# Performance work log

Hardware: AMD Instinct MI355X
Metric: run time of the kernel (lower is better)

Reference implementation:

```python
import jax, jax.numpy as jnp
import numpy as np

NUM_FIELDS = 26

def setup_inputs() -> dict:
    key = jax.random.key(0)
    ks = jax.random.split(key, 8)
    B, F, D, V, d, af = 4096, NUM_FIELDS, 13, 100000, 64, 64
    return {
        "sparse_feat": jax.random.randint(ks[0], (B, F), 0, V, dtype=jnp.int32),
        "dense_feat": jax.random.uniform(ks[1], (B, D), dtype=jnp.float32),
        "embed_table": jax.random.normal(ks[2], (V, d), dtype=jnp.float32) * 0.05,
        "lin_table": jax.random.normal(ks[3], (V,), dtype=jnp.float32) * 0.05,
        "w_dense": jax.random.normal(ks[4], (D,), dtype=jnp.float32) * 0.1,
        "bias": jnp.zeros((1,), dtype=jnp.float32),
        "W1": jax.random.normal(ks[5], (d, af), dtype=jnp.float32) * (1.0 / np.sqrt(d)),
        "b1": jnp.zeros((af,), dtype=jnp.float32),
        "w2": jax.random.normal(ks[6], (af,), dtype=jnp.float32) * (1.0 / np.sqrt(af)),
        "p": jax.random.normal(ks[7], (d,), dtype=jnp.float32) * (1.0 / np.sqrt(d)),
    }

def reference(sparse_feat, dense_feat, embed_table, lin_table, w_dense, bias, W1, b1, w2, p):
    # Embedding lookup: [B, F, d]
    emb = embed_table[sparse_feat]
    # Linear part: per-field scalar weights + dense linear + bias -> [B]
    linear_out = lin_table[sparse_feat].sum(axis=1) + dense_feat @ w_dense + bias[0]
    # Pairwise interactions i<j (static indices): [B, P, d]
    i_idx, j_idx = np.triu_indices(NUM_FIELDS, k=1)
    att_x = emb[:, i_idx, :] * emb[:, j_idx, :]
    # Attention MLP: Linear(d, af) + ReLU + Linear(af, 1, no bias) -> [B, P]
    h = jax.nn.relu(jnp.einsum('bpd,da->bpa', att_x, W1) + b1)
    att_w = jnp.einsum('bpa,a->bp', h, w2)
    att_score = jax.nn.softmax(att_w, axis=1)
    # Softmax-weighted sum over pairs -> [B, d], then final projection p -> [B]
    att_out = jnp.einsum('bpd,bp->bd', att_x, att_score)
    fm_att_out = att_out @ p
    return linear_out + fm_att_out
```

## Files before the change

kernel.cpp:

```cpp
#include <hip/hip_runtime.h>
#include <math.h>


#define NF 26
#define NP 325
#define NMT 21
#define ED 64
#define AF 64
#define NDENSE 13
#define WPB 4
#define BLOCK (WPB * 64)
#define ESTRIDE 72
#define EBYTES (ESTRIDE * 2)

typedef __attribute__((ext_vector_type(8))) _Float16 half8;
typedef __attribute__((ext_vector_type(4))) float f32x4;

__device__ __forceinline__ void wsync() {
    __builtin_amdgcn_fence(__ATOMIC_ACQ_REL, "workgroup");
    __builtin_amdgcn_wave_barrier();
}

__global__ void prep_kernel(const float* __restrict__ W1,
                            _Float16* __restrict__ w1t,
                            unsigned short* __restrict__ ptab)
{
    int t = threadIdx.x;
    for (int idx = t; idx < ED * AF; idx += 256) {
        int d = idx >> 6, a = idx & 63;
        w1t[a * ED + d] = (_Float16)W1[idx];
    }
    if (t < 16 * 24) {
        int ln = t / 24, mt = t % 24;
        int p = mt * 16 + ln;
        unsigned short v = 0;
        if (mt < NMT && p < NP) {
            int rem = p, i = 0;
            while (rem >= NF - 1 - i) { rem -= NF - 1 - i; ++i; }
            v = (unsigned short)(i | ((i + 1 + rem) << 8));
        }
        ptab[t] = v;
    }
}

__global__ __launch_bounds__(BLOCK, 4)
void afm_kernel(const int*   __restrict__ sparse,
                const float* __restrict__ dense,
                const float* __restrict__ etab,
                const float* __restrict__ ltab,
                const float* __restrict__ wdense,
                const float* __restrict__ bias,
                const float* __restrict__ b1,
                const float* __restrict__ w2,
                const float* __restrict__ proj,
                const _Float16* __restrict__ w1t,
                const unsigned*  __restrict__ ptab32,
                float*       __restrict__ out,
                int B)
{
    const int t    = threadIdx.x;
    const int wave = t >> 6;
    const int lane = t & 63;
    const int qd   = lane >> 4;
    const int ln   = lane & 15;

    const int r = blockIdx.x * WPB + wave;
    if (r >= B) return;

    __shared__ alignas(16) _Float16 emb_all[WPB][NF][ESTRIDE];
    _Float16 (* __restrict__ emb)[ESTRIDE] = emb_all[wave];
    const char* __restrict__ ebase = (const char*)emb;

    half8 bfr[4][2];
    #pragma unroll
    for (int nt = 0; nt < 4; ++nt)
        #pragma unroll
        for (int kh = 0; kh < 2; ++kh)
            bfr[nt][kh] = *(const half8*)(w1t + (nt * 16 + ln) * ED + kh * 32 + qd * 8);

    float4 b1v4[4], w2v4[4];
    #pragma unroll
    for (int nt = 0; nt < 4; ++nt) {
        b1v4[nt] = *(const float4*)(b1 + nt * 16 + qd * 4);
        w2v4[nt] = *(const float4*)(w2 + nt * 16 + qd * 4);
    }

    unsigned pt[12];
    {
        const unsigned* myp = ptab32 + ln * 12;
        #pragma unroll
        for (int w = 0; w < 12; ++w) pt[w] = myp[w];
    }

    const int* __restrict__ srow = sparse + r * NF;
    for (int task = lane; task < NF * 8; task += 64) {
        int f = task >> 3, c = task & 7;
        const float* src = etab + (size_t)srow[f] * ED + c * 8;
        float4 v0 = *(const float4*)(src);
        float4 v1 = *(const float4*)(src + 4);
        half8 h = { (_Float16)v0.x, (_Float16)v0.y, (_Float16)v0.z, (_Float16)v0.w,
                    (_Float16)v1.x, (_Float16)v1.y, (_Float16)v1.z, (_Float16)v1.w };
        *(half8*)(&emb[f][c * 8]) = h;
    }

    float lin = 0.f;
    if (lane < NF) {
        lin = ltab[srow[lane]];
    } else if (lane >= 32 && lane < 32 + NDENSE) {
        int k = lane - 32;
        lin = dense[r * NDENSE + k] * wdense[k];
    }
    #pragma unroll
    for (int off = 32; off >= 1; off >>= 1) lin += __shfl_xor(lin, off, 64);
    lin += bias[0];

    wsync();

    float l = 0.f;
    half8 acc0 = { (_Float16)0.f, (_Float16)0.f, (_Float16)0.f, (_Float16)0.f,
                   (_Float16)0.f, (_Float16)0.f, (_Float16)0.f, (_Float16)0.f };
    half8 acc1 = acc0;

    #pragma unroll
    for (int mt = 0; mt < NMT; ++mt) {
        const unsigned pk = (pt[mt >> 1] >> ((mt & 1) << 4)) & 0xffffu;
        const int oi = (int)(pk & 0xffu) * EBYTES;
        const int oj = (int)(pk >> 8) * EBYTES;

        half8 ei0 = *(const half8*)(ebase + oi + qd * 16);
        half8 ei1 = *(const half8*)(ebase + oi + 64 + qd * 16);
        half8 ej0 = *(const half8*)(ebase + oj + qd * 16);
        half8 ej1 = *(const half8*)(ebase + oj + 64 + qd * 16);
        half8 x0 = ei0 * ej0;
        half8 x1 = ei1 * ej1;

        float lg = 0.f;
        #pragma unroll
        for (int nt = 0; nt < 4; ++nt) {
            f32x4 acc = { b1v4[nt].x, b1v4[nt].y, b1v4[nt].z, b1v4[nt].w };
            acc = __builtin_amdgcn_mfma_f32_16x16x32_f16(bfr[nt][0], x0, acc, 0, 0, 0);
            acc = __builtin_amdgcn_mfma_f32_16x16x32_f16(bfr[nt][1], x1, acc, 0, 0, 0);
            lg = fmaf(fmaxf(acc[0], 0.f), w2v4[nt].x, lg);
            lg = fmaf(fmaxf(acc[1], 0.f), w2v4[nt].y, lg);
            lg = fmaf(fmaxf(acc[2], 0.f), w2v4[nt].z, lg);
            lg = fmaf(fmaxf(acc[3], 0.f), w2v4[nt].w, lg);
        }
        lg += __shfl_xor(lg, 16, 64);
        lg += __shfl_xor(lg, 32, 64);

        float e = (mt * 16 + ln < NP) ? __expf(lg) : 0.f;
        l += e;
        const _Float16 eh = (_Float16)e;
        half8 e8 = { eh, eh, eh, eh, eh, eh, eh, eh };
        acc0 += x0 * e8;
        acc1 += x1 * e8;
    }

    float lsum = l;
    #pragma unroll
    for (int off = 1; off <= 8; off <<= 1) lsum += __shfl_xor(lsum, off, 64);

    float4 pa = *(const float4*)(proj + qd * 8);
    float4 pb = *(const float4*)(proj + qd * 8 + 4);
    float4 pc = *(const float4*)(proj + 32 + qd * 8);
    float4 pd = *(const float4*)(proj + 32 + qd * 8 + 4);
    float rr = (float)acc0[0] * pa.x + (float)acc0[1] * pa.y
             + (float)acc0[2] * pa.z + (float)acc0[3] * pa.w
             + (float)acc0[4] * pb.x + (float)acc0[5] * pb.y
             + (float)acc0[6] * pb.z + (float)acc0[7] * pb.w
             + (float)acc1[0] * pc.x + (float)acc1[1] * pc.y
             + (float)acc1[2] * pc.z + (float)acc1[3] * pc.w
             + (float)acc1[4] * pd.x + (float)acc1[5] * pd.y
             + (float)acc1[6] * pd.z + (float)acc1[7] * pd.w;
    #pragma unroll
    for (int off = 1; off <= 32; off <<= 1) rr += __shfl_xor(rr, off, 64);

    if (lane == 0) out[r] = lin + rr / lsum;
}

extern "C" void kernel_launch(void* const* d_in, const int* in_sizes, int n_in,
                              void* d_out, int out_size, void* d_ws, size_t ws_size,
                              hipStream_t stream) {
    const int*   sparse = (const int*)  d_in[0];
    const float* dense  = (const float*)d_in[1];
    const float* etab   = (const float*)d_in[2];
    const float* ltab   = (const float*)d_in[3];
    const float* wdense = (const float*)d_in[4];
    const float* bias   = (const float*)d_in[5];
    const float* W1     = (const float*)d_in[6];
    const float* b1     = (const float*)d_in[7];
    const float* w2     = (const float*)d_in[8];
    const float* proj   = (const float*)d_in[9];
    float* outp = (float*)d_out;

    _Float16*       w1t  = (_Float16*)d_ws;
    unsigned short* ptab = (unsigned short*)((char*)d_ws + 8192);

    const int B = in_sizes[0] / NF;

    prep_kernel<<<dim3(1), dim3(256), 0, stream>>>(W1, w1t, ptab);
    afm_kernel<<<dim3((B + WPB - 1) / WPB), dim3(BLOCK), 0, stream>>>(
        sparse, dense, etab, ltab, wdense, bias, b1, w2, proj, w1t,
        (const unsigned*)ptab, outp, B);
    (void)n_in; (void)out_size; (void)ws_size;
}
```

Measured before the change: 120.6 us.

## Process two rows per wave, drop prep kernel, compute pair indices inline

Removes the separate prep kernel. W1 is now converted to fp16 fragments directly from global memory inside the main kernel, and the pair-index table is replaced by a closed-form sqrt computation of (i,j) per pair. Each wave now handles two batch rows. The second row's embedding gather is issued after the first row's setup so it can overlap with compute, and the per-wave W1/b1/w2 fragment loads are amortized over both rows. The changes trade an extra launch and table loads for strided W1 loads, inline sqrt math, doubled shared memory per block and half as many blocks.

```diff
diff --git a/kernel.cpp b/kernel.cpp
--- a/kernel.cpp
+++ b/kernel.cpp
@@ -10,6 +10,7 @@
 #define NDENSE 13
 #define WPB 4
 #define BLOCK (WPB * 64)
+#define RPW 2
 #define ESTRIDE 72
 #define EBYTES (ESTRIDE * 2)
 
@@ -19,28 +20,6 @@
 __device__ __forceinline__ void wsync() {
     __builtin_amdgcn_fence(__ATOMIC_ACQ_REL, "workgroup");
     __builtin_amdgcn_wave_barrier();
-}
-
-__global__ void prep_kernel(const float* __restrict__ W1,
-                            _Float16* __restrict__ w1t,
-                            unsigned short* __restrict__ ptab)
-{
-    int t = threadIdx.x;
-    for (int idx = t; idx < ED * AF; idx += 256) {
-        int d = idx >> 6, a = idx & 63;
-        w1t[a * ED + d] = (_Float16)W1[idx];
-    }
-    if (t < 16 * 24) {
-        int ln = t / 24, mt = t % 24;
-        int p = mt * 16 + ln;
-        unsigned short v = 0;
-        if (mt < NMT && p < NP) {
-            int rem = p, i = 0;
-            while (rem >= NF - 1 - i) { rem -= NF - 1 - i; ++i; }
-            v = (unsigned short)(i | ((i + 1 + rem) << 8));
-        }
-        ptab[t] = v;
-    }
 }
 
 __global__ __launch_bounds__(BLOCK, 4)
@@ -50,11 +29,10 @@
                 const float* __restrict__ ltab,
                 const float* __restrict__ wdense,
                 const float* __restrict__ bias,
+                const float* __restrict__ W1,
                 const float* __restrict__ b1,
                 const float* __restrict__ w2,
                 const float* __restrict__ proj,
-                const _Float16* __restrict__ w1t,
-                const unsigned*  __restrict__ ptab32,
                 float*       __restrict__ out,
                 int B)
 {
@@ -64,19 +42,25 @@
     const int qd   = lane >> 4;
     const int ln   = lane & 15;
 
-    const int r = blockIdx.x * WPB + wave;
-    if (r >= B) return;
-
-    __shared__ alignas(16) _Float16 emb_all[WPB][NF][ESTRIDE];
-    _Float16 (* __restrict__ emb)[ESTRIDE] = emb_all[wave];
-    const char* __restrict__ ebase = (const char*)emb;
+    const int g  = blockIdx.x * WPB + wave;
+    const int r0 = g * RPW;
+    if (r0 >= B) return;
+    const int r1 = r0 + 1;
+
+    __shared__ alignas(16) _Float16 emb_all[WPB][RPW][NF][ESTRIDE];
+    const char* __restrict__ ebase0 = (const char*)&emb_all[wave][0][0][0];
 
     half8 bfr[4][2];
     #pragma unroll
     for (int nt = 0; nt < 4; ++nt)
         #pragma unroll
-        for (int kh = 0; kh < 2; ++kh)
-            bfr[nt][kh] = *(const half8*)(w1t + (nt * 16 + ln) * ED + kh * 32 + qd * 8);
+        for (int kh = 0; kh < 2; ++kh) {
+            const float* wp = W1 + (kh * 32 + qd * 8) * AF + nt * 16 + ln;
+            half8 h;
+            #pragma unroll
+            for (int j = 0; j < 8; ++j) h[j] = (_Float16)wp[j * AF];
+            bfr[nt][kh] = h;
+        }
 
     float4 b1v4[4], w2v4[4];
     #pragma unroll
@@ -85,97 +69,125 @@
         w2v4[nt] = *(const float4*)(w2 + nt * 16 + qd * 4);
     }
 
-    unsigned pt[12];
-    {
-        const unsigned* myp = ptab32 + ln * 12;
-        #pragma unroll
-        for (int w = 0; w < 12; ++w) pt[w] = myp[w];
-    }
-
-    const int* __restrict__ srow = sparse + r * NF;
+    const int* __restrict__ srow0 = sparse + r0 * NF;
+    const int* __restrict__ srow1 = sparse + r1 * NF;
     for (int task = lane; task < NF * 8; task += 64) {
         int f = task >> 3, c = task & 7;
-        const float* src = etab + (size_t)srow[f] * ED + c * 8;
+        const float* src = etab + (size_t)srow0[f] * ED + c * 8;
         float4 v0 = *(const float4*)(src);
         float4 v1 = *(const float4*)(src + 4);
         half8 h = { (_Float16)v0.x, (_Float16)v0.y, (_Float16)v0.z, (_Float16)v0.w,
                     (_Float16)v1.x, (_Float16)v1.y, (_Float16)v1.z, (_Float16)v1.w };
-        *(half8*)(&emb[f][c * 8]) = h;
-    }
-
-    float lin = 0.f;
+        *(half8*)(&emb_all[wave][0][f][c * 8]) = h;
+    }
+
+    float lin0 = 0.f, lin1 = 0.f;
     if (lane < NF) {
-        lin = ltab[srow[lane]];
+        lin0 = ltab[srow0[lane]];
+        if (r1 < B) lin1 = ltab[srow1[lane]];
     } else if (lane >= 32 && lane < 32 + NDENSE) {
         int k = lane - 32;
-        lin = dense[r * NDENSE + k] * wdense[k];
+        lin0 = dense[r0 * NDENSE + k] * wdense[k];
+        if (r1 < B) lin1 = dense[r1 * NDENSE + k] * wdense[k];
     }
     #pragma unroll
-    for (int off = 32; off >= 1; off >>= 1) lin += __shfl_xor(lin, off, 64);
-    lin += bias[0];
+    for (int off = 32; off >= 1; off >>= 1) {
+        lin0 += __shfl_xor(lin0, off, 64);
+        lin1 += __shfl_xor(lin1, off, 64);
+    }
+    const float bb = bias[0];
+    lin0 += bb; lin1 += bb;
 
     wsync();
 
-    float l = 0.f;
-    half8 acc0 = { (_Float16)0.f, (_Float16)0.f, (_Float16)0.f, (_Float16)0.f,
-                   (_Float16)0.f, (_Float16)0.f, (_Float16)0.f, (_Float16)0.f };
-    half8 acc1 = acc0;
-
-    #pragma unroll
-    for (int mt = 0; mt < NMT; ++mt) {
-        const unsigned pk = (pt[mt >> 1] >> ((mt & 1) << 4)) & 0xffffu;
-        const int oi = (int)(pk & 0xffu) * EBYTES;
-        const int oj = (int)(pk >> 8) * EBYTES;
-
-        half8 ei0 = *(const half8*)(ebase + oi + qd * 16);
-        half8 ei1 = *(const half8*)(ebase + oi + 64 + qd * 16);
-        half8 ej0 = *(const half8*)(ebase + oj + qd * 16);
-        half8 ej1 = *(const half8*)(ebase + oj + 64 + qd * 16);
-        half8 x0 = ei0 * ej0;
-        half8 x1 = ei1 * ej1;
-
-        float lg = 0.f;
-        #pragma unroll
-        for (int nt = 0; nt < 4; ++nt) {
-            f32x4 acc = { b1v4[nt].x, b1v4[nt].y, b1v4[nt].z, b1v4[nt].w };
-            acc = __builtin_amdgcn_mfma_f32_16x16x32_f16(bfr[nt][0], x0, acc, 0, 0, 0);
-            acc = __builtin_amdgcn_mfma_f32_16x16x32_f16(bfr[nt][1], x1, acc, 0, 0, 0);
-            lg = fmaf(fmaxf(acc[0], 0.f), w2v4[nt].x, lg);
-            lg = fmaf(fmaxf(acc[1], 0.f), w2v4[nt].y, lg);
-            lg = fmaf(fmaxf(acc[2], 0.f), w2v4[nt].z, lg);
-            lg = fmaf(fmaxf(acc[3], 0.f), w2v4[nt].w, lg);
+    if (r1 < B) {
+        for (int task = lane; task < NF * 8; task += 64) {
+            int f = task >> 3, c = task & 7;
+            const float* src = etab + (size_t)srow1[f] * ED + c * 8;
+            float4 v0 = *(const float4*)(src);
+            float4 v1 = *(const float4*)(src + 4);
+            half8 h = { (_Float16)v0.x, (_Float16)v0.y, (_Float16)v0.z, (_Float16)v0.w,
+                        (_Float16)v1.x, (_Float16)v1.y, (_Float16)v1.z, (_Float16)v1.w };
+            *(half8*)(&emb_all[wave][1][f][c * 8]) = h;
         }
-        lg += __shfl_xor(lg, 16, 64);
-        lg += __shfl_xor(lg, 32, 64);
-
-        float e = (mt * 16 + ln < NP) ? __expf(lg) : 0.f;
-        l += e;
-        const _Float16 eh = (_Float16)e;
-        half8 e8 = { eh, eh, eh, eh, eh, eh, eh, eh };
-        acc0 += x0 * e8;
-        acc1 += x1 * e8;
-    }
-
-    float lsum = l;
-    #pragma unroll
-    for (int off = 1; off <= 8; off <<= 1) lsum += __shfl_xor(lsum, off, 64);
-
-    float4 pa = *(const float4*)(proj + qd * 8);
-    float4 pb = *(const float4*)(proj + qd * 8 + 4);
-    float4 pc = *(const float4*)(proj + 32 + qd * 8);
-    float4 pd = *(const float4*)(proj + 32 + qd * 8 + 4);
-    float rr = (float)acc0[0] * pa.x + (float)acc0[1] * pa.y
-             + (float)acc0[2] * pa.z + (float)acc0[3] * pa.w
-             + (float)acc0[4] * pb.x + (float)acc0[5] * pb.y
-             + (float)acc0[6] * pb.z + (float)acc0[7] * pb.w
-             + (float)acc1[0] * pc.x + (float)acc1[1] * pc.y
-             + (float)acc1[2] * pc.z + (float)acc1[3] * pc.w
-             + (float)acc1[4] * pd.x + (float)acc1[5] * pd.y
-             + (float)acc1[6] * pd.z + (float)acc1[7] * pd.w;
-    #pragma unroll
-    for (int off = 1; off <= 32; off <<= 1) rr += __shfl_xor(rr, off, 64);
-
-    if (lane == 0) out[r] = lin + rr / lsum;
+    }
+
+    const int qo0 = qd * 16;
+    const int qo1 = 64 + qd * 16;
+
+    #pragma unroll 1
+    for (int rr = 0; rr < RPW; ++rr) {
+        const int r = r0 + rr;
+        if (r >= B) break;
+        if (rr) wsync();
+        const char* __restrict__ ebase = ebase0 + rr * (NF * EBYTES);
+
+        float l = 0.f;
+        half8 acc0 = { (_Float16)0.f, (_Float16)0.f, (_Float16)0.f, (_Float16)0.f,
+                       (_Float16)0.f, (_Float16)0.f, (_Float16)0.f, (_Float16)0.f };
+        half8 acc1 = acc0;
+
+        #pragma unroll
+        for (int mt = 0; mt < NMT; ++mt) {
+            const int p  = mt * 16 + ln;
+            const int pc = (p < NP) ? p : 0;
+            const float sq = sqrtf((float)(2601 - 8 * pc));
+            const int fi = (int)((51.0f - sq) * 0.5f);
+            const int fj = fi + 1 + pc - ((fi * (51 - fi)) >> 1);
+            const int oi = fi * EBYTES, oj = fj * EBYTES;
+
+            half8 ei0 = *(const half8*)(ebase + oi + qo0);
+            half8 ei1 = *(const half8*)(ebase + oi + qo1);
+            half8 ej0 = *(const half8*)(ebase + oj + qo0);
+            half8 ej1 = *(const half8*)(ebase + oj + qo1);
+            half8 x0 = ei0 * ej0;
+            half8 x1 = ei1 * ej1;
+
+            float lgA = 0.f, lgB = 0.f;
+            #pragma unroll
+            for (int nt = 0; nt < 4; ++nt) {
+                f32x4 acc = { b1v4[nt].x, b1v4[nt].y, b1v4[nt].z, b1v4[nt].w };
+                acc = __builtin_amdgcn_mfma_f32_16x16x32_f16(bfr[nt][0], x0, acc, 0, 0, 0);
+                acc = __builtin_amdgcn_mfma_f32_16x16x32_f16(bfr[nt][1], x1, acc, 0, 0, 0);
+                float s0 = fmaf(fmaxf(acc[0], 0.f), w2v4[nt].x,
+                                fmaxf(acc[1], 0.f) * w2v4[nt].y);
+                float s1 = fmaf(fmaxf(acc[2], 0.f), w2v4[nt].z,
+                                fmaxf(acc[3], 0.f) * w2v4[nt].w);
+                if (nt & 1) lgB += s0 + s1; else lgA += s0 + s1;
+            }
+            float lg = lgA + lgB;
+            lg += __shfl_xor(lg, 16, 64);
+            lg += __shfl_xor(lg, 32, 64);
+
+            float e = (p < NP) ? __expf(lg) : 0.f;
+            l += e;
+            const _Float16 eh = (_Float16)e;
+            half8 e8 = { eh, eh, eh, eh, eh, eh, eh, eh };
+            acc0 += x0 * e8;
+            acc1 += x1 * e8;
+        }
+
+        float lsum = l;
+        #pragma unroll
+        for (int off = 1; off <= 8; off <<= 1) lsum += __shfl_xor(lsum, off, 64);
+
+        float4 pa = *(const float4*)(proj + qd * 8);
+        float4 pb = *(const float4*)(proj + qd * 8 + 4);
+        float4 pc4 = *(const float4*)(proj + 32 + qd * 8);
+        float4 pd = *(const float4*)(proj + 32 + qd * 8 + 4);
+        float rrv = (float)acc0[0] * pa.x + (float)acc0[1] * pa.y
+                  + (float)acc0[2] * pa.z + (float)acc0[3] * pa.w
+                  + (float)acc0[4] * pb.x + (float)acc0[5] * pb.y
+                  + (float)acc0[6] * pb.z + (float)acc0[7] * pb.w
+                  + (float)acc1[0] * pc4.x + (float)acc1[1] * pc4.y
+                  + (float)acc1[2] * pc4.z + (float)acc1[3] * pc4.w
+                  + (float)acc1[4] * pd.x + (float)acc1[5] * pd.y
+                  + (float)acc1[6] * pd.z + (float)acc1[7] * pd.w;
+        #pragma unroll
+        for (int off = 1; off <= 32; off <<= 1) rrv += __shfl_xor(rrv, off, 64);
+
+        if (lane == 0) out[r] = ((rr == 0) ? lin0 : lin1) + rrv / lsum;
+    }
 }
 
 extern "C" void kernel_launch(void* const* d_in, const int* in_sizes, int n_in,
@@ -193,14 +205,11 @@
     const float* proj   = (const float*)d_in[9];
     float* outp = (float*)d_out;
 
-    _Float16*       w1t  = (_Float16*)d_ws;
-    unsigned short* ptab = (unsigned short*)((char*)d_ws + 8192);
-
     const int B = in_sizes[0] / NF;
-
-    prep_kernel<<<dim3(1), dim3(256), 0, stream>>>(W1, w1t, ptab);
-    afm_kernel<<<dim3((B + WPB - 1) / WPB), dim3(BLOCK), 0, stream>>>(
-        sparse, dense, etab, ltab, wdense, bias, b1, w2, proj, w1t,
-        (const unsigned*)ptab, outp, B);
-    (void)n_in; (void)out_size; (void)ws_size;
+    const int rows_per_block = WPB * RPW;
+    const int grid = (B + rows_per_block - 1) / rows_per_block;
+
+    afm_kernel<<<dim3(grid), dim3(BLOCK), 0, stream>>>(
+        sparse, dense, etab, ltab, wdense, bias, W1, b1, w2, proj, outp, B);
+    (void)n_in; (void)out_size; (void)ws_size; (void)d_ws;
 }
```

Measured after the change: 129.0 us. +7.0%, slower.

## Split each row's pair tiles across two waves and compute pair indices analytically

Applied to the files above, without the earlier changes.

Each block now handles a single batch row with two waves that take alternating 16-pair tiles, instead of one wave per row with four rows per block. The two waves' partial softmax sums and projected outputs are merged through shared memory after a block barrier. The precomputed pair lookup table is replaced by a closed-form sqrt-based (i,j) computation, which removes the table and its per-lane loads. This doubles the wave count to hide gather and MFMA latency, at the cost of block-level barriers, one fully masked extra tile, and some extra per-tile arithmetic.

```diff
diff --git a/kernel.cpp b/kernel.cpp
--- a/kernel.cpp
+++ b/kernel.cpp
@@ -8,38 +8,20 @@
 #define ED 64
 #define AF 64
 #define NDENSE 13
-#define WPB 4
-#define BLOCK (WPB * 64)
+#define BLOCK 128
 #define ESTRIDE 72
 #define EBYTES (ESTRIDE * 2)
 
 typedef __attribute__((ext_vector_type(8))) _Float16 half8;
 typedef __attribute__((ext_vector_type(4))) float f32x4;
 
-__device__ __forceinline__ void wsync() {
-    __builtin_amdgcn_fence(__ATOMIC_ACQ_REL, "workgroup");
-    __builtin_amdgcn_wave_barrier();
-}
-
 __global__ void prep_kernel(const float* __restrict__ W1,
-                            _Float16* __restrict__ w1t,
-                            unsigned short* __restrict__ ptab)
+                            _Float16* __restrict__ w1t)
 {
     int t = threadIdx.x;
     for (int idx = t; idx < ED * AF; idx += 256) {
         int d = idx >> 6, a = idx & 63;
         w1t[a * ED + d] = (_Float16)W1[idx];
-    }
-    if (t < 16 * 24) {
-        int ln = t / 24, mt = t % 24;
-        int p = mt * 16 + ln;
-        unsigned short v = 0;
-        if (mt < NMT && p < NP) {
-            int rem = p, i = 0;
-            while (rem >= NF - 1 - i) { rem -= NF - 1 - i; ++i; }
-            v = (unsigned short)(i | ((i + 1 + rem) << 8));
-        }
-        ptab[t] = v;
     }
 }
 
@@ -54,21 +36,17 @@
                 const float* __restrict__ w2,
                 const float* __restrict__ proj,
                 const _Float16* __restrict__ w1t,
-                const unsigned*  __restrict__ ptab32,
-                float*       __restrict__ out,
-                int B)
+                float*       __restrict__ out)
 {
     const int t    = threadIdx.x;
     const int wave = t >> 6;
     const int lane = t & 63;
     const int qd   = lane >> 4;
     const int ln   = lane & 15;
+    const int r    = blockIdx.x;
 
-    const int r = blockIdx.x * WPB + wave;
-    if (r >= B) return;
-
-    __shared__ alignas(16) _Float16 emb_all[WPB][NF][ESTRIDE];
-    _Float16 (* __restrict__ emb)[ESTRIDE] = emb_all[wave];
+    __shared__ alignas(16) _Float16 emb[NF][ESTRIDE];
+    __shared__ float merge[2][2];
     const char* __restrict__ ebase = (const char*)emb;
 
     half8 bfr[4][2];
@@ -85,15 +63,8 @@
         w2v4[nt] = *(const float4*)(w2 + nt * 16 + qd * 4);
     }
 
-    unsigned pt[12];
-    {
-        const unsigned* myp = ptab32 + ln * 12;
-        #pragma unroll
-        for (int w = 0; w < 12; ++w) pt[w] = myp[w];
-    }
-
     const int* __restrict__ srow = sparse + r * NF;
-    for (int task = lane; task < NF * 8; task += 64) {
+    for (int task = t; task < NF * 8; task += BLOCK) {
         int f = task >> 3, c = task & 7;
         const float* src = etab + (size_t)srow[f] * ED + c * 8;
         float4 v0 = *(const float4*)(src);
@@ -104,17 +75,22 @@
     }
 
     float lin = 0.f;
-    if (lane < NF) {
-        lin = ltab[srow[lane]];
-    } else if (lane >= 32 && lane < 32 + NDENSE) {
-        int k = lane - 32;
-        lin = dense[r * NDENSE + k] * wdense[k];
+    if (wave == 0) {
+        if (lane < NF) {
+            lin = ltab[srow[lane]];
+        } else if (lane >= 32 && lane < 32 + NDENSE) {
+            int k = lane - 32;
+            lin = dense[r * NDENSE + k] * wdense[k];
+        }
+        #pragma unroll
+        for (int off = 32; off >= 1; off >>= 1) lin += __shfl_xor(lin, off, 64);
+        lin += bias[0];
     }
-    #pragma unroll
-    for (int off = 32; off >= 1; off >>= 1) lin += __shfl_xor(lin, off, 64);
-    lin += bias[0];
 
-    wsync();
+    __syncthreads();
+
+    const int qo0 = qd * 16;
+    const int qo1 = 64 + qd * 16;
 
     float l = 0.f;
     half8 acc0 = { (_Float16)0.f, (_Float16)0.f, (_Float16)0.f, (_Float16)0.f,
@@ -122,15 +98,19 @@
     half8 acc1 = acc0;
 
     #pragma unroll
-    for (int mt = 0; mt < NMT; ++mt) {
-        const unsigned pk = (pt[mt >> 1] >> ((mt & 1) << 4)) & 0xffffu;
-        const int oi = (int)(pk & 0xffu) * EBYTES;
-        const int oj = (int)(pk >> 8) * EBYTES;
+    for (int k = 0; k < 11; ++k) {
+        const int mt = 2 * k + wave;
+        const int p  = mt * 16 + ln;
+        const int pc = (p < NP) ? p : 0;
+        const float sq = sqrtf((float)(2601 - 8 * pc));
+        const int fi = (int)((51.0f - sq) * 0.5f);
+        const int fj = fi + 1 + pc - ((fi * (51 - fi)) >> 1);
+        const int oi = fi * EBYTES, oj = fj * EBYTES;
 
-        half8 ei0 = *(const half8*)(ebase + oi + qd * 16);
-        half8 ei1 = *(const half8*)(ebase + oi + 64 + qd * 16);
-        half8 ej0 = *(const half8*)(ebase + oj + qd * 16);
-        half8 ej1 = *(const half8*)(ebase + oj + 64 + qd * 16);
+        half8 ei0 = *(const half8*)(ebase + oi + qo0);
+        half8 ei1 = *(const half8*)(ebase + oi + qo1);
+        half8 ej0 = *(const half8*)(ebase + oj + qo0);
+        half8 ej1 = *(const half8*)(ebase + oj + qo1);
         half8 x0 = ei0 * ej0;
         half8 x1 = ei1 * ej1;
 
@@ -148,7 +128,7 @@
         lg += __shfl_xor(lg, 16, 64);
         lg += __shfl_xor(lg, 32, 64);
 
-        float e = (mt * 16 + ln < NP) ? __expf(lg) : 0.f;
+        float e = (p < NP) ? __expf(lg) : 0.f;
         l += e;
         const _Float16 eh = (_Float16)e;
         half8 e8 = { eh, eh, eh, eh, eh, eh, eh, eh };
@@ -162,20 +142,25 @@
 
     float4 pa = *(const float4*)(proj + qd * 8);
     float4 pb = *(const float4*)(proj + qd * 8 + 4);
-    float4 pc = *(const float4*)(proj + 32 + qd * 8);
+    float4 pc4 = *(const float4*)(proj + 32 + qd * 8);
     float4 pd = *(const float4*)(proj + 32 + qd * 8 + 4);
-    float rr = (float)acc0[0] * pa.x + (float)acc0[1] * pa.y
-             + (float)acc0[2] * pa.z + (float)acc0[3] * pa.w
-             + (float)acc0[4] * pb.x + (float)acc0[5] * pb.y
-             + (float)acc0[6] * pb.z + (float)acc0[7] * pb.w
-             + (float)acc1[0] * pc.x + (float)acc1[1] * pc.y
-             + (float)acc1[2] * pc.z + (float)acc1[3] * pc.w
-             + (float)acc1[4] * pd.x + (float)acc1[5] * pd.y
-             + (float)acc1[6] * pd.z + (float)acc1[7] * pd.w;
+    float rrv = (float)acc0[0] * pa.x + (float)acc0[1] * pa.y
+              + (float)acc0[2] * pa.z + (float)acc0[3] * pa.w
+              + (float)acc0[4] * pb.x + (float)acc0[5] * pb.y
+              + (float)acc0[6] * pb.z + (float)acc0[7] * pb.w
+              + (float)acc1[0] * pc4.x + (float)acc1[1] * pc4.y
+              + (float)acc1[2] * pc4.z + (float)acc1[3] * pc4.w
+              + (float)acc1[4] * pd.x + (float)acc1[5] * pd.y
+              + (float)acc1[6] * pd.z + (float)acc1[7] * pd.w;
     #pragma unroll
-    for (int off = 1; off <= 32; off <<= 1) rr += __shfl_xor(rr, off, 64);
+    for (int off = 1; off <= 32; off <<= 1) rrv += __shfl_xor(rrv, off, 64);
 
-    if (lane == 0) out[r] = lin + rr / lsum;
+    if (lane == 0) { merge[wave][0] = rrv; merge[wave][1] = lsum; }
+
+    __syncthreads();
+
+    if (t == 0)
+        out[r] = lin + (merge[0][0] + merge[1][0]) / (merge[0][1] + merge[1][1]);
 }
 
 extern "C" void kernel_launch(void* const* d_in, const int* in_sizes, int n_in,
@@ -193,14 +178,12 @@
     const float* proj   = (const float*)d_in[9];
     float* outp = (float*)d_out;
 
-    _Float16*       w1t  = (_Float16*)d_ws;
-    unsigned short* ptab = (unsigned short*)((char*)d_ws + 8192);
+    _Float16* w1t = (_Float16*)d_ws;
 
     const int B = in_sizes[0] / NF;
 
-    prep_kernel<<<dim3(1), dim3(256), 0, stream>>>(W1, w1t, ptab);
-    afm_kernel<<<dim3((B + WPB - 1) / WPB), dim3(BLOCK), 0, stream>>>(
-        sparse, dense, etab, ltab, wdense, bias, b1, w2, proj, w1t,
-        (const unsigned*)ptab, outp, B);
+    prep_kernel<<<dim3(1), dim3(256), 0, stream>>>(W1, w1t);
+    afm_kernel<<<dim3(B), dim3(BLOCK), 0, stream>>>(
+        sparse, dense, etab, ltab, wdense, bias, b1, w2, proj, w1t, outp);
     (void)n_in; (void)out_size; (void)ws_size;
 }
```

Result: no change. 120.1 us (-0.5%).
